# Optimization experiments

Hardware: AMD Instinct MI355X
Metric: run time of the kernel (lower is better)

Reference implementation:

```python
import jax, jax.numpy as jnp
import numpy as np

EPS = 1e-5

def layer_norm(x, g, b):
    mu = jnp.mean(x, axis=-1, keepdims=True)
    var = jnp.mean(jnp.square(x - mu), axis=-1, keepdims=True)
    return (x - mu) * jax.lax.rsqrt(var + EPS) * g + b

def setup_inputs() -> dict:
    key = jax.random.key(0)
    ks = jax.random.split(key, 8)
    B, T, D, H = 8, 2048, 32, 4
    hd = D // H
    s = 0.05
    return {
        "x": jax.random.normal(ks[0], (B, T, D), jnp.float32),
        "Wq": jax.random.normal(ks[1], (H, D, hd), jnp.float32) * s,
        "Wk": jax.random.normal(ks[2], (H, D, hd), jnp.float32) * s,
        "Wv": jax.random.normal(ks[3], (H, D, hd), jnp.float32) * s,
        "Wproj": jax.random.normal(ks[4], (D, D), jnp.float32) * s,
        "bproj": jnp.zeros((D,), jnp.float32),
        "ln1_g": jnp.ones((D,), jnp.float32),
        "ln1_b": jnp.zeros((D,), jnp.float32),
        "W1": jax.random.normal(ks[5], (D, 4 * D), jnp.float32) * s,
        "b1": jnp.zeros((4 * D,), jnp.float32),
        "W2": jax.random.normal(ks[6], (4 * D, D), jnp.float32) * s,
        "b2": jnp.zeros((D,), jnp.float32),
        "ln2_g": jnp.ones((D,), jnp.float32),
        "ln2_b": jnp.zeros((D,), jnp.float32),
    }

def reference(x, Wq, Wk, Wv, Wproj, bproj, ln1_g, ln1_b, W1, b1, W2, b2, ln2_g, ln2_b):
    B, T, D = x.shape
    H, _, hd = Wq.shape
    scale = hd ** -0.5
    # NOTE: original block normalizes first, and the residual uses the NORMALIZED x
    h = layer_norm(x, ln1_g, ln1_b)                      # (B,T,D)
    q = jnp.einsum('btd,hdk->bhtk', h, Wq)
    k = jnp.einsum('btd,hdk->bhtk', h, Wk)
    v = jnp.einsum('btd,hdk->bhtk', h, Wv)
    scores = jnp.einsum('bhtk,bhsk->bhts', q, k) * scale  # (B,H,T,T)
    mask = jnp.tril(jnp.ones((T, T), bool))
    scores = jnp.where(mask, scores, -jnp.inf)
    attn = jax.nn.softmax(scores, axis=-1)               # dropout = identity (eval)
    o = jnp.einsum('bhts,bhsk->bhtk', attn, v)           # (B,H,T,hd)
    o = o.transpose(0, 2, 1, 3).reshape(B, T, D)         # concat heads, head0 first
    x1 = h + o @ Wproj + bproj
    h2 = layer_norm(x1, ln2_g, ln2_b)
    ff = jax.nn.relu(h2 @ W1 + b1) @ W2 + b2             # dropout = identity (eval)
    return h2 + ff
```

## Files before the change

### kernel.cpp

```cpp
#include <hip/hip_runtime.h>
#include <math.h>

#define BB 8
#define TT 2048
#define DD 32
#define HH 4
#define HD 8
#define NROWS (BB*TT)
#define LNEPS 1e-5f

#if __has_builtin(__builtin_amdgcn_exp2f)
#define EXP2F(x) __builtin_amdgcn_exp2f(x)
#else
#define EXP2F(x) __expf(0.6931471805599453f*(x))
#endif

typedef _Float16 h2 __attribute__((ext_vector_type(2)));
typedef _Float16 h4v __attribute__((ext_vector_type(4)));
typedef float f4v __attribute__((ext_vector_type(4)));
struct KH { h2 a, b, c, d; };
union F4H { float4 f; KH k; };

static __device__ __forceinline__ h2 pkrtz(float a, float b) {
    return __builtin_bit_cast(h2, __builtin_amdgcn_cvt_pkrtz(a, b));
}
static __device__ __forceinline__ unsigned pkrtz_u(float a, float b) {
    return __builtin_bit_cast(unsigned, __builtin_amdgcn_cvt_pkrtz(a, b));
}
static __device__ __forceinline__ unsigned short f16u(float x) {
    return __builtin_bit_cast(unsigned short, (_Float16)x);
}

__global__ __launch_bounds__(256) void k_ln_qkv(
    const float* __restrict__ x,
    const float* __restrict__ Wq, const float* __restrict__ Wk, const float* __restrict__ Wv,
    const float* __restrict__ g, const float* __restrict__ b,
    float* __restrict__ h, float* __restrict__ qh,
    float* __restrict__ Kh, float* __restrict__ Vt)
{
    __shared__ float sW[3*HH*264];
    __shared__ float sg[DD], sb[DD];
    for (int i = threadIdx.x; i < HH*DD*HD; i += 256) {
        int hd_ = i >> 8, off = i & 255;
        sW[hd_*264 + off]              = Wq[i];
        sW[(4+hd_)*264 + off]          = Wk[i];
        sW[(8+hd_)*264 + off]          = Wv[i];
    }
    if (threadIdx.x < DD) { sg[threadIdx.x] = g[threadIdx.x]; sb[threadIdx.x] = b[threadIdx.x]; }
    __syncthreads();

    int idx = blockIdx.x * 256 + threadIdx.x;
    int r   = idx >> 3;
    int sub = idx & 7;
    int hh  = sub & 3;
    int dh  = sub >> 2;
    int bb  = r >> 11, tt = r & 2047;

    float xr[16];
    {
        const float4* xp = (const float4*)(x + (size_t)r * DD + dh*16);
        float4 t0 = xp[0], t1 = xp[1], t2 = xp[2], t3 = xp[3];
        xr[0]=t0.x; xr[1]=t0.y; xr[2]=t0.z; xr[3]=t0.w;
        xr[4]=t1.x; xr[5]=t1.y; xr[6]=t1.z; xr[7]=t1.w;
        xr[8]=t2.x; xr[9]=t2.y; xr[10]=t2.z; xr[11]=t2.w;
        xr[12]=t3.x; xr[13]=t3.y; xr[14]=t3.z; xr[15]=t3.w;
    }
    float s1 = 0.f;
    #pragma unroll
    for (int i = 0; i < 16; ++i) s1 += xr[i];
    s1 += __shfl_xor(s1, 4, 64);
    float mu = s1 * (1.f/DD);
    float sq = 0.f;
    #pragma unroll
    for (int i = 0; i < 16; ++i) { float d = xr[i]-mu; sq += d*d; }
    sq += __shfl_xor(sq, 4, 64);
    float rs = rsqrtf(sq * (1.f/DD) + LNEPS);

    float hr[16];
    #pragma unroll
    for (int i = 0; i < 16; ++i) hr[i] = (xr[i]-mu)*rs*sg[dh*16+i] + sb[dh*16+i];

    {
        float4* hp = (float4*)(h + (size_t)r * DD + dh*16);
        hp[0]=make_float4(hr[0],hr[1],hr[2],hr[3]);
        hp[1]=make_float4(hr[4],hr[5],hr[6],hr[7]);
        hp[2]=make_float4(hr[8],hr[9],hr[10],hr[11]);
        hp[3]=make_float4(hr[12],hr[13],hr[14],hr[15]);
    }

    const float* wq = sW + hh*264 + dh*128;
    const float* wk = sW + (4+hh)*264 + dh*128;
    const float* wv = sW + (8+hh)*264 + dh*128;
    float qa[HD], ka[HD], va[HD];
    #pragma unroll
    for (int k2 = 0; k2 < HD; ++k2) { qa[k2]=0.f; ka[k2]=0.f; va[k2]=0.f; }
    #pragma unroll
    for (int d = 0; d < 16; ++d) {
        float hv = hr[d];
        const float4* wq4 = (const float4*)(wq + d*8);
        const float4* wk4 = (const float4*)(wk + d*8);
        const float4* wv4 = (const float4*)(wv + d*8);
        float4 a0 = wq4[0], a1 = wq4[1];
        float4 b0 = wk4[0], b1 = wk4[1];
        float4 c0 = wv4[0], c1 = wv4[1];
        qa[0]=fmaf(hv,a0.x,qa[0]); qa[1]=fmaf(hv,a0.y,qa[1]); qa[2]=fmaf(hv,a0.z,qa[2]); qa[3]=fmaf(hv,a0.w,qa[3]);
        qa[4]=fmaf(hv,a1.x,qa[4]); qa[5]=fmaf(hv,a1.y,qa[5]); qa[6]=fmaf(hv,a1.z,qa[6]); qa[7]=fmaf(hv,a1.w,qa[7]);
        ka[0]=fmaf(hv,b0.x,ka[0]); ka[1]=fmaf(hv,b0.y,ka[1]); ka[2]=fmaf(hv,b0.z,ka[2]); ka[3]=fmaf(hv,b0.w,ka[3]);
        ka[4]=fmaf(hv,b1.x,ka[4]); ka[5]=fmaf(hv,b1.y,ka[5]); ka[6]=fmaf(hv,b1.z,ka[6]); ka[7]=fmaf(hv,b1.w,ka[7]);
        va[0]=fmaf(hv,c0.x,va[0]); va[1]=fmaf(hv,c0.y,va[1]); va[2]=fmaf(hv,c0.z,va[2]); va[3]=fmaf(hv,c0.w,va[3]);
        va[4]=fmaf(hv,c1.x,va[4]); va[5]=fmaf(hv,c1.y,va[5]); va[6]=fmaf(hv,c1.z,va[6]); va[7]=fmaf(hv,c1.w,va[7]);
    }
    #pragma unroll
    for (int k2 = 0; k2 < HD; ++k2) {
        qa[k2] += __shfl_xor(qa[k2], 4, 64);
        ka[k2] += __shfl_xor(ka[k2], 4, 64);
        va[k2] += __shfl_xor(va[k2], 4, 64);
    }

    const float SCL = 0.35355339059327373f * 1.4426950408889634f;
    size_t key = (size_t)(bb*HH + hh)*TT + tt;
    unsigned short* vtb = (unsigned short*)Vt + (size_t)(bb*HH + hh)*8*TT + tt;
    if (dh == 0) {
        F4H u;
        u.k.a = pkrtz(qa[0]*SCL, qa[1]*SCL);
        u.k.b = pkrtz(qa[2]*SCL, qa[3]*SCL);
        u.k.c = pkrtz(qa[4]*SCL, qa[5]*SCL);
        u.k.d = pkrtz(qa[6]*SCL, qa[7]*SCL);
        *(float4*)(qh + key*4) = u.f;
        vtb[(size_t)0*TT] = f16u(va[0]);
        vtb[(size_t)1*TT] = f16u(va[1]);
        vtb[(size_t)2*TT] = f16u(va[2]);
        vtb[(size_t)3*TT] = f16u(va[3]);
    } else {
        F4H u;
        u.k.a = pkrtz(ka[0], ka[1]);
        u.k.b = pkrtz(ka[2], ka[3]);
        u.k.c = pkrtz(ka[4], ka[5]);
        u.k.d = pkrtz(ka[6], ka[7]);
        *(float4*)(Kh + key*4) = u.f;
        vtb[(size_t)4*TT] = f16u(va[4]);
        vtb[(size_t)5*TT] = f16u(va[5]);
        vtb[(size_t)6*TT] = f16u(va[6]);
        vtb[(size_t)7*TT] = f16u(va[7]);
    }
}

__global__ __launch_bounds__(256) void k_attn(
    const float* __restrict__ qh, const float* __restrict__ Kh,
    const float* __restrict__ Vt, float* __restrict__ o)
{
    __shared__ char lds[2][2048];
    const int tid  = threadIdx.x;
    const int wave = tid >> 6;
    const int lane = tid & 63;
    const int g    = lane >> 4;
    const int qi   = lane & 15;
    const int bh   = blockIdx.x & 31;
    const int qblk = 31 - (int)(blockIdx.x >> 5);
    const int qb   = qblk << 6;
    const int wq0  = qb + (wave << 4);
    const int ntiles = qblk + 1;

    const float4*  KbF = (const float4*)Kh + (size_t)bh * TT;
    const ushort*  VtU = (const ushort*)Vt + (size_t)bh * 8 * TT;

    h4v qf;
    {
        uint2 qraw = make_uint2(0u, 0u);
        if (g < 2)
            qraw = *(const uint2*)((const ushort*)qh + ((size_t)bh*TT + wq0 + qi)*8 + (size_t)(g<<2));
        qf = __builtin_bit_cast(h4v, qraw);
    }

    f4v acc = {0.f, 0.f, 0.f, 0.f};
    float m = 0.f, l = 0.f;

    float4 st = make_float4(0.f,0.f,0.f,0.f);
    if (tid < 64) {
        st = KbF[tid];
    } else if (tid < 128) {
        int t2 = tid - 64, d = t2 >> 3, seg = (t2 & 7) ^ d;
        st = *(const float4*)(VtU + (size_t)d*TT + (seg << 3));
    }
    if (tid < 64)       *(float4*)(&lds[0][0] + tid*16) = st;
    else if (tid < 128) *(float4*)(&lds[0][0] + 1024 + (tid-64)*16) = st;
    __syncthreads();

    int buf = 0;
    for (int t = 0; t < ntiles; ++t) {
        const int tb = t << 6;
        float4 nx = make_float4(0.f,0.f,0.f,0.f);
        const bool more = (t + 1 < ntiles);
        if (more) {
            const int nb = (t + 1) << 6;
            if (tid < 64) nx = KbF[nb + tid];
            else if (tid < 128) {
                int t2 = tid - 64, d = t2 >> 3, seg = (t2 & 7) ^ d;
                nx = *(const float4*)(VtU + (size_t)d*TT + nb + (seg << 3));
            }
        }
        const char* smK = &lds[buf][0];
        const char* smV = &lds[buf][0] + 1024;
        #pragma unroll
        for (int c = 0; c < 4; ++c) {
            const int s0 = tb + (c << 4);
            if (s0 > wq0) continue;
            const bool diag = (s0 == wq0);

            uint2 kraw = *(const uint2*)(smK + ((c<<4) + qi)*16 + ((g&1)<<3));
            if (g >= 2) { kraw.x = 0u; kraw.y = 0u; }
            h4v kf = __builtin_bit_cast(h4v, kraw);

            const int d7 = lane & 7;
            uint2 vraw = *(const uint2*)(smV + d7*128 + (((c<<5) + (g<<3)) ^ (d7<<4)));
            h4v vf = __builtin_bit_cast(h4v, vraw);

            f4v Z = {0.f,0.f,0.f,0.f};
            f4v S = __builtin_amdgcn_mfma_f32_16x16x16f16(kf, qf, Z, 0, 0, 0);

            float dd[4];
            #pragma unroll
            for (int r = 0; r < 4; ++r) {
                float v = S[r];
                if (diag && ((g<<2) + r > qi)) v = -1e30f;
                dd[r] = v;
            }
            float pm = fmaxf(fmaxf(dd[0], dd[1]), fmaxf(dd[2], dd[3]));
            pm = fmaxf(pm, __shfl_xor(pm, 16, 64));
            pm = fmaxf(pm, __shfl_xor(pm, 32, 64));
            if (__builtin_expect(__any(pm - m > 8.f), 0)) {
                float mn = fmaxf(m, pm);
                float cr = EXP2F(m - mn);
                l *= cr;
                #pragma unroll
                for (int r = 0; r < 4; ++r) {
                    float c4 = __shfl(cr, (g<<2) + r, 64);
                    acc[r] *= c4;
                }
                m = mn;
            }
            float p0 = EXP2F(dd[0] - m);
            float p1 = EXP2F(dd[1] - m);
            float p2 = EXP2F(dd[2] - m);
            float p3 = EXP2F(dd[3] - m);
            l += (p0 + p1) + (p2 + p3);
            uint2 pu; pu.x = pkrtz_u(p0, p1); pu.y = pkrtz_u(p2, p3);
            h4v pf = __builtin_bit_cast(h4v, pu);
            acc = __builtin_amdgcn_mfma_f32_16x16x16f16(pf, vf, acc, 0, 0, 0);
        }
        if (more) {
            if (tid < 64)       *(float4*)(&lds[buf^1][0] + tid*16) = nx;
            else if (tid < 128) *(float4*)(&lds[buf^1][0] + 1024 + (tid-64)*16) = nx;
        }
        __syncthreads();
        buf ^= 1;
    }

    l += __shfl_xor(l, 16, 64);
    l += __shfl_xor(l, 32, 64);
    float Linv = 1.f / l;
    float Li[4];
    #pragma unroll
    for (int r = 0; r < 4; ++r) Li[r] = __shfl(Linv, (g<<2) + r, 64);
    if (qi < HD) {
        float* ob = o + ((size_t)bh*TT + wq0)*HD + qi;
        #pragma unroll
        for (int r = 0; r < 4; ++r)
            ob[(size_t)((g<<2) + r) * HD] = acc[r] * Li[r];
    }
}

__global__ __launch_bounds__(256) void k_proj_ffn(
    const float* __restrict__ h, const float* __restrict__ o,
    const float* __restrict__ Wproj, const float* __restrict__ bproj,
    const float* __restrict__ W1, const float* __restrict__ b1,
    const float* __restrict__ W2, const float* __restrict__ b2,
    const float* __restrict__ g2, const float* __restrict__ bt2,
    float* __restrict__ out)
{
    __shared__ float sWp[DD*36], sW1T[4*DD*36], sW2[4*DD*36];
    __shared__ float sbp[DD], sb1[4*DD], sb2[DD], sg2[DD], sbt2[DD];
    for (int i = threadIdx.x; i < DD*DD; i += 256)      sWp [(i>>5)*36 + (i&31)] = Wproj[i];
    for (int i = threadIdx.x; i < DD*4*DD; i += 256) {
        sW1T[(i&127)*36 + (i>>7)] = W1[i];
        sW2 [(i>>5)*36 + (i&31)]  = W2[i];
    }
    if (threadIdx.x < DD) {
        sbp[threadIdx.x]  = bproj[threadIdx.x];
        sb2[threadIdx.x]  = b2[threadIdx.x];
        sg2[threadIdx.x]  = g2[threadIdx.x];
        sbt2[threadIdx.x] = bt2[threadIdx.x];
    }
    if (threadIdx.x < 4*DD) sb1[threadIdx.x] = b1[threadIdx.x];
    __syncthreads();

    int idx = blockIdx.x * 256 + threadIdx.x;
    int r   = idx >> 3;
    int sub = idx & 7;
    int bb  = r >> 11, tt = r & 2047;

    float o4[4];
    #pragma unroll
    for (int mm = 0; mm < 4; ++mm)
        o4[mm] = o[((size_t)(bb*HH + mm)*TT + tt) * HD + sub];

    float x1[DD];
    #pragma unroll
    for (int d = 0; d < DD; ++d) x1[d] = 0.f;
    #pragma unroll
    for (int mm = 0; mm < 4; ++mm) {
        const float4* wr = (const float4*)&sWp[(sub + 8*mm)*36];
        float ov = o4[mm];
        #pragma unroll
        for (int dc = 0; dc < 8; ++dc) {
            float4 w4 = wr[dc];
            x1[4*dc]   = fmaf(ov, w4.x, x1[4*dc]);
            x1[4*dc+1] = fmaf(ov, w4.y, x1[4*dc+1]);
            x1[4*dc+2] = fmaf(ov, w4.z, x1[4*dc+2]);
            x1[4*dc+3] = fmaf(ov, w4.w, x1[4*dc+3]);
        }
    }
    #pragma unroll
    for (int d = 0; d < DD; ++d) {
        x1[d] += __shfl_xor(x1[d], 1, 64);
        x1[d] += __shfl_xor(x1[d], 2, 64);
        x1[d] += __shfl_xor(x1[d], 4, 64);
    }
    {
        const float4* hp = (const float4*)(h + (size_t)r * DD);
        #pragma unroll
        for (int dc = 0; dc < 8; ++dc) {
            float4 h4 = hp[dc];
            x1[4*dc]   += h4.x + sbp[4*dc];
            x1[4*dc+1] += h4.y + sbp[4*dc+1];
            x1[4*dc+2] += h4.z + sbp[4*dc+2];
            x1[4*dc+3] += h4.w + sbp[4*dc+3];
        }
    }
    float mu = 0.f;
    #pragma unroll
    for (int d = 0; d < DD; ++d) mu += x1[d];
    mu *= (1.f/DD);
    float var = 0.f;
    #pragma unroll
    for (int d = 0; d < DD; ++d) { float dl = x1[d]-mu; var += dl*dl; }
    var *= (1.f/DD);
    float rs = rsqrtf(var + LNEPS);
    float h2v[DD];
    #pragma unroll
    for (int d = 0; d < DD; ++d) h2v[d] = (x1[d]-mu)*rs*sg2[d] + sbt2[d];

    float outp[DD];
    #pragma unroll
    for (int d = 0; d < DD; ++d) outp[d] = 0.f;
    #pragma unroll
    for (int mm = 0; mm < 16; ++mm) {
        int j = sub + 8*mm;
        const float4* w1r = (const float4*)&sW1T[j*36];
        float a = sb1[j];
        #pragma unroll
        for (int dc = 0; dc < 8; ++dc) {
            float4 w4 = w1r[dc];
            a = fmaf(h2v[4*dc], w4.x, a);
            a = fmaf(h2v[4*dc+1], w4.y, a);
            a = fmaf(h2v[4*dc+2], w4.z, a);
            a = fmaf(h2v[4*dc+3], w4.w, a);
        }
        a = fmaxf(a, 0.f);
        const float4* w2r = (const float4*)&sW2[j*36];
        #pragma unroll
        for (int dc = 0; dc < 8; ++dc) {
            float4 w4 = w2r[dc];
            outp[4*dc]   = fmaf(a, w4.x, outp[4*dc]);
            outp[4*dc+1] = fmaf(a, w4.y, outp[4*dc+1]);
            outp[4*dc+2] = fmaf(a, w4.z, outp[4*dc+2]);
            outp[4*dc+3] = fmaf(a, w4.w, outp[4*dc+3]);
        }
    }
    if (sub == 0) {
        #pragma unroll
        for (int d = 0; d < DD; ++d) outp[d] += h2v[d] + sb2[d];
    }
    float t1[16];
    #pragma unroll
    for (int i = 0; i < 16; ++i) {
        bool hi = (sub & 4) != 0;
        float send = hi ? outp[i] : outp[i+16];
        float recv = __shfl_xor(send, 4, 64);
        t1[i] = (hi ? outp[i+16] : outp[i]) + recv;
    }
    float t2[8];
    #pragma unroll
    for (int i = 0; i < 8; ++i) {
        bool hi = (sub & 2) != 0;
        float send = hi ? t1[i] : t1[i+8];
        float recv = __shfl_xor(send, 2, 64);
        t2[i] = (hi ? t1[i+8] : t1[i]) + recv;
    }
    float w0[4];
    #pragma unroll
    for (int i = 0; i < 4; ++i) {
        bool hi = (sub & 1) != 0;
        float send = hi ? t2[i] : t2[i+4];
        float recv = __shfl_xor(send, 1, 64);
        w0[i] = (hi ? t2[i+4] : t2[i]) + recv;
    }
    *(float4*)(out + (size_t)r * DD + sub*4) = make_float4(w0[0], w0[1], w0[2], w0[3]);
}

extern "C" void kernel_launch(void* const* d_in, const int* in_sizes, int n_in,
                              void* d_out, int out_size, void* d_ws, size_t ws_size,
                              hipStream_t stream) {
    const float* x     = (const float*)d_in[0];
    const float* Wq    = (const float*)d_in[1];
    const float* Wk    = (const float*)d_in[2];
    const float* Wv    = (const float*)d_in[3];
    const float* Wproj = (const float*)d_in[4];
    const float* bproj = (const float*)d_in[5];
    const float* ln1_g = (const float*)d_in[6];
    const float* ln1_b = (const float*)d_in[7];
    const float* W1    = (const float*)d_in[8];
    const float* b1    = (const float*)d_in[9];
    const float* W2    = (const float*)d_in[10];
    const float* b2    = (const float*)d_in[11];
    const float* ln2_g = (const float*)d_in[12];
    const float* ln2_b = (const float*)d_in[13];
    float* out = (float*)d_out;

    const size_t N = (size_t)NROWS * DD;
    const size_t K = (size_t)BB*HH*TT*4;
    float* ws = (float*)d_ws;
    float* h  = ws;
    float* qh = ws + N;
    float* Kh = ws + N + K;
    float* Vt = ws + N + 2*K;
    float* o  = ws + N + 3*K;

    k_ln_qkv  <<<512, 256, 0, stream>>>(x, Wq, Wk, Wv, ln1_g, ln1_b, h, qh, Kh, Vt);
    k_attn    <<<1024, 256, 0, stream>>>(qh, Kh, Vt, o);
    k_proj_ffn<<<512, 256, 0, stream>>>(h, o, Wproj, bproj, W1, b1, W2, b2, ln2_g, ln2_b, out);
}
```

Baseline: 137.9 us.

## Switch attention to 32x32 MFMA tiles with split-K waves and merged softmax

The attention kernel moves from 16x16x16 MFMA with half-wasted lanes to 32x32x8 for scores and 32x32x16 for P·V, so each wave handles 32 queries. The four waves now pair up: each pair shares a query group and alternates key tiles, then merges max, sum and partial outputs through LDS at the end. K and V are written in a new tiled, swizzled layout to match. The running max is folded into the MFMA accumulator input, and row sums use fdot2. This aims to reduce wasted MFMA work and softmax overhead per key, at the cost of a cross-wave merge and extra synchronisation.

```diff
diff --git a/kernel.cpp b/kernel.cpp
--- a/kernel.cpp
+++ b/kernel.cpp
@@ -17,7 +17,8 @@
 
 typedef _Float16 h2 __attribute__((ext_vector_type(2)));
 typedef _Float16 h4v __attribute__((ext_vector_type(4)));
-typedef float f4v __attribute__((ext_vector_type(4)));
+typedef _Float16 h8v __attribute__((ext_vector_type(8)));
+typedef float f32x16 __attribute__((ext_vector_type(16)));
 struct KH { h2 a, b, c, d; };
 union F4H { float4 f; KH k; };
 
@@ -30,6 +31,12 @@
 static __device__ __forceinline__ unsigned short f16u(float x) {
     return __builtin_bit_cast(unsigned short, (_Float16)x);
 }
+
+#if __has_builtin(__builtin_amdgcn_fdot2)
+#define DOT2(a,b,c) __builtin_amdgcn_fdot2((a),(b),(c),false)
+#else
+#define DOT2(a,b,c) fmaf((float)(a)[1],(float)(b)[1], fmaf((float)(a)[0],(float)(b)[0],(c)))
+#endif
 
 __global__ __launch_bounds__(256) void k_ln_qkv(
     const float* __restrict__ x,
@@ -119,7 +126,9 @@
 
     const float SCL = 0.35355339059327373f * 1.4426950408889634f;
     size_t key = (size_t)(bb*HH + hh)*TT + tt;
-    unsigned short* vtb = (unsigned short*)Vt + (size_t)(bb*HH + hh)*8*TT + tt;
+    char* Vb8 = (char*)Vt + (size_t)(bb*HH + hh)*32768;
+    int t6 = tt >> 6, tr = (tt & 63) << 1;
+    char* vrow = Vb8 + t6*128;
     if (dh == 0) {
         F4H u;
         u.k.a = pkrtz(qa[0]*SCL, qa[1]*SCL);
@@ -127,146 +136,204 @@
         u.k.c = pkrtz(qa[4]*SCL, qa[5]*SCL);
         u.k.d = pkrtz(qa[6]*SCL, qa[7]*SCL);
         *(float4*)(qh + key*4) = u.f;
-        vtb[(size_t)0*TT] = f16u(va[0]);
-        vtb[(size_t)1*TT] = f16u(va[1]);
-        vtb[(size_t)2*TT] = f16u(va[2]);
-        vtb[(size_t)3*TT] = f16u(va[3]);
+        *(unsigned short*)(vrow + 0*4096 + (tr ^ 0))   = f16u(va[0]);
+        *(unsigned short*)(vrow + 1*4096 + (tr ^ 16))  = f16u(va[1]);
+        *(unsigned short*)(vrow + 2*4096 + (tr ^ 32))  = f16u(va[2]);
+        *(unsigned short*)(vrow + 3*4096 + (tr ^ 48))  = f16u(va[3]);
     } else {
-        F4H u;
-        u.k.a = pkrtz(ka[0], ka[1]);
-        u.k.b = pkrtz(ka[2], ka[3]);
-        u.k.c = pkrtz(ka[4], ka[5]);
-        u.k.d = pkrtz(ka[6], ka[7]);
-        *(float4*)(Kh + key*4) = u.f;
-        vtb[(size_t)4*TT] = f16u(va[4]);
-        vtb[(size_t)5*TT] = f16u(va[5]);
-        vtb[(size_t)6*TT] = f16u(va[6]);
-        vtb[(size_t)7*TT] = f16u(va[7]);
-    }
+        char* Kb8 = (char*)Kh + (size_t)(bb*HH + hh)*32768;
+        uint2 k01; k01.x = pkrtz_u(ka[0],ka[1]); k01.y = pkrtz_u(ka[2],ka[3]);
+        uint2 k23; k23.x = pkrtz_u(ka[4],ka[5]); k23.y = pkrtz_u(ka[6],ka[7]);
+        *(uint2*)(Kb8 + (size_t)tt*8) = k01;
+        *(uint2*)(Kb8 + 16384 + (size_t)tt*8) = k23;
+        *(unsigned short*)(vrow + 4*4096 + (tr ^ 64))  = f16u(va[4]);
+        *(unsigned short*)(vrow + 5*4096 + (tr ^ 80))  = f16u(va[5]);
+        *(unsigned short*)(vrow + 6*4096 + (tr ^ 96))  = f16u(va[6]);
+        *(unsigned short*)(vrow + 7*4096 + (tr ^ 112)) = f16u(va[7]);
+    }
+}
+
+template<bool DIAG>
+__device__ __forceinline__ void do_chunk(
+    const char* __restrict__ smK, const char* __restrict__ smV,
+    int kc, int hi, int col, h4v qf,
+    float& m, float& l, f32x16& acc)
+{
+    uint2 kraw = *(const uint2*)(smK + hi*512 + (size_t)(kc + col)*8);
+    h4v kf = __builtin_bit_cast(h4v, kraw);
+    f32x16 cin;
+    #pragma unroll
+    for (int r2 = 0; r2 < 16; ++r2) cin[r2] = -m;
+    f32x16 S = __builtin_amdgcn_mfma_f32_32x32x8f16(kf, qf, cin, 0, 0, 0);
+    if (DIAG) {
+        #pragma unroll
+        for (int r2 = 0; r2 < 16; ++r2) {
+            int row = (r2&3) + 8*(r2>>2) + 4*hi;
+            if (row > col) S[r2] = -1e30f;
+        }
+    }
+    float pm = S[0];
+    #pragma unroll
+    for (int r2 = 1; r2 < 16; ++r2) pm = fmaxf(pm, S[r2]);
+    pm = fmaxf(pm, __shfl_xor(pm, 32, 64));
+    if (__builtin_expect(__any(pm > 8.f), 0)) {
+        float adj = fmaxf(pm, 0.f);
+        float cr  = EXP2F(-adj);
+        l *= cr;
+        #pragma unroll
+        for (int r2 = 0; r2 < 16; ++r2) {
+            int row = (r2&3) + 8*(r2>>2) + 4*hi;
+            acc[r2] *= __shfl(cr, row, 64);
+        }
+        #pragma unroll
+        for (int r2 = 0; r2 < 16; ++r2) S[r2] -= adj;
+        m += adj;
+    }
+    float p[16];
+    #pragma unroll
+    for (int r2 = 0; r2 < 16; ++r2) p[r2] = EXP2F(S[r2]);
+    unsigned pa_ = pkrtz_u(p[0],  p[1]);
+    unsigned pb_ = pkrtz_u(p[2],  p[3]);
+    unsigned pc_ = pkrtz_u(p[4],  p[5]);
+    unsigned pd_ = pkrtz_u(p[6],  p[7]);
+    unsigned pe_ = pkrtz_u(p[8],  p[9]);
+    unsigned pf_ = pkrtz_u(p[10], p[11]);
+    unsigned pg_ = pkrtz_u(p[12], p[13]);
+    unsigned ph_ = pkrtz_u(p[14], p[15]);
+    const h2 one2 = {(_Float16)1.f, (_Float16)1.f};
+    l = DOT2(__builtin_bit_cast(h2, pa_), one2, l);
+    l = DOT2(__builtin_bit_cast(h2, pb_), one2, l);
+    l = DOT2(__builtin_bit_cast(h2, pc_), one2, l);
+    l = DOT2(__builtin_bit_cast(h2, pd_), one2, l);
+    l = DOT2(__builtin_bit_cast(h2, pe_), one2, l);
+    l = DOT2(__builtin_bit_cast(h2, pf_), one2, l);
+    l = DOT2(__builtin_bit_cast(h2, pg_), one2, l);
+    l = DOT2(__builtin_bit_cast(h2, ph_), one2, l);
+    unsigned ra = (unsigned)__shfl_xor((int)pa_, 32, 64);
+    unsigned rb = (unsigned)__shfl_xor((int)pb_, 32, 64);
+    unsigned rc = (unsigned)__shfl_xor((int)pc_, 32, 64);
+    unsigned rd = (unsigned)__shfl_xor((int)pd_, 32, 64);
+    unsigned re = (unsigned)__shfl_xor((int)pe_, 32, 64);
+    unsigned rf = (unsigned)__shfl_xor((int)pf_, 32, 64);
+    unsigned rg = (unsigned)__shfl_xor((int)pg_, 32, 64);
+    unsigned rh = (unsigned)__shfl_xor((int)ph_, 32, 64);
+    bool H = (hi != 0);
+    uint4 A0 = { H?rc:pa_, H?rd:pb_, H?pc_:ra, H?pd_:rb };
+    uint4 A1 = { H?rg:pe_, H?rh:pf_, H?pg_:re, H?ph_:rf };
+    int d7 = col & 7;
+    const char* vrow = smV + d7*128;
+    uint4 v0 = *(const uint4*)(vrow + ((((kc + hi*8) << 1)) ^ (d7 << 4)));
+    uint4 v1 = *(const uint4*)(vrow + ((((kc + 16 + hi*8) << 1)) ^ (d7 << 4)));
+    acc = __builtin_amdgcn_mfma_f32_32x32x16_f16(
+        __builtin_bit_cast(h8v, A0), __builtin_bit_cast(h8v, v0), acc, 0, 0, 0);
+    acc = __builtin_amdgcn_mfma_f32_32x32x16_f16(
+        __builtin_bit_cast(h8v, A1), __builtin_bit_cast(h8v, v1), acc, 0, 0, 0);
 }
 
 __global__ __launch_bounds__(256) void k_attn(
     const float* __restrict__ qh, const float* __restrict__ Kh,
     const float* __restrict__ Vt, float* __restrict__ o)
 {
-    __shared__ char lds[2][2048];
+    __shared__ char lds[7168];
     const int tid  = threadIdx.x;
     const int wave = tid >> 6;
     const int lane = tid & 63;
-    const int g    = lane >> 4;
-    const int qi   = lane & 15;
+    const int hi   = lane >> 5;
+    const int col  = lane & 31;
+    const int qg   = wave >> 1;
+    const int kh   = wave & 1;
     const int bh   = blockIdx.x & 31;
     const int qblk = 31 - (int)(blockIdx.x >> 5);
     const int qb   = qblk << 6;
-    const int wq0  = qb + (wave << 4);
+    const int wq0  = qb + (qg << 5);
     const int ntiles = qblk + 1;
 
-    const float4*  KbF = (const float4*)Kh + (size_t)bh * TT;
-    const ushort*  VtU = (const ushort*)Vt + (size_t)bh * 8 * TT;
-
-    h4v qf;
+    const char* Kg = (const char*)Kh + (size_t)bh * 32768;
+    const char* Vg = (const char*)Vt + (size_t)bh * 32768;
+    const char* Qg = (const char*)qh + (size_t)bh * 32768 + (size_t)wq0 * 16;
+
+    h4v qf = __builtin_bit_cast(h4v, *(const uint2*)(Qg + col*16 + hi*8));
+
+    f32x16 acc;
+    #pragma unroll
+    for (int r2 = 0; r2 < 16; ++r2) acc[r2] = 0.f;
+    float m = 0.f, l = 0.f;
+
     {
-        uint2 qraw = make_uint2(0u, 0u);
-        if (g < 2)
-            qraw = *(const uint2*)((const ushort*)qh + ((size_t)bh*TT + wq0 + qi)*8 + (size_t)(g<<2));
-        qf = __builtin_bit_cast(h4v, qraw);
-    }
-
-    f4v acc = {0.f, 0.f, 0.f, 0.f};
-    float m = 0.f, l = 0.f;
-
-    float4 st = make_float4(0.f,0.f,0.f,0.f);
-    if (tid < 64) {
-        st = KbF[tid];
-    } else if (tid < 128) {
-        int t2 = tid - 64, d = t2 >> 3, seg = (t2 & 7) ^ d;
-        st = *(const float4*)(VtU + (size_t)d*TT + (seg << 3));
-    }
-    if (tid < 64)       *(float4*)(&lds[0][0] + tid*16) = st;
-    else if (tid < 128) *(float4*)(&lds[0][0] + 1024 + (tid-64)*16) = st;
+        uint4 st;
+        if (tid < 64)       st = *(const uint4*)(Kg + (tid>>5)*16384 + (size_t)(tid&31)*16);
+        else if (tid < 128) { int ix = tid-64; st = *(const uint4*)(Vg + (ix>>3)*4096 + (ix&7)*16); }
+        if (tid < 64)       *(uint4*)(&lds[0] + (tid>>5)*512 + (tid&31)*16) = st;
+        else if (tid < 128) *(uint4*)(&lds[0] + 1024 + (tid-64)*16) = st;
+    }
     __syncthreads();
 
     int buf = 0;
     for (int t = 0; t < ntiles; ++t) {
-        const int tb = t << 6;
-        float4 nx = make_float4(0.f,0.f,0.f,0.f);
+        uint4 nx;
         const bool more = (t + 1 < ntiles);
         if (more) {
-            const int nb = (t + 1) << 6;
-            if (tid < 64) nx = KbF[nb + tid];
-            else if (tid < 128) {
-                int t2 = tid - 64, d = t2 >> 3, seg = (t2 & 7) ^ d;
-                nx = *(const float4*)(VtU + (size_t)d*TT + nb + (seg << 3));
+            if (tid < 64)       nx = *(const uint4*)(Kg + (tid>>5)*16384 + (t+1)*512 + (tid&31)*16);
+            else if (tid < 128) { int ix = tid-64; nx = *(const uint4*)(Vg + (ix>>3)*4096 + (t+1)*128 + (ix&7)*16); }
+        }
+        if ((t & 1) == kh) {
+            const int tb = t << 6;
+            const char* smK = &lds[buf*2048];
+            const char* smV = smK + 1024;
+            if (tb <= wq0) {
+                if (tb == wq0) do_chunk<true >(smK, smV, 0, hi, col, qf, m, l, acc);
+                else           do_chunk<false>(smK, smV, 0, hi, col, qf, m, l, acc);
+                if (tb + 32 <= wq0) {
+                    if (tb + 32 == wq0) do_chunk<true >(smK, smV, 32, hi, col, qf, m, l, acc);
+                    else                do_chunk<false>(smK, smV, 32, hi, col, qf, m, l, acc);
+                }
             }
         }
-        const char* smK = &lds[buf][0];
-        const char* smV = &lds[buf][0] + 1024;
-        #pragma unroll
-        for (int c = 0; c < 4; ++c) {
-            const int s0 = tb + (c << 4);
-            if (s0 > wq0) continue;
-            const bool diag = (s0 == wq0);
-
-            uint2 kraw = *(const uint2*)(smK + ((c<<4) + qi)*16 + ((g&1)<<3));
-            if (g >= 2) { kraw.x = 0u; kraw.y = 0u; }
-            h4v kf = __builtin_bit_cast(h4v, kraw);
-
-            const int d7 = lane & 7;
-            uint2 vraw = *(const uint2*)(smV + d7*128 + (((c<<5) + (g<<3)) ^ (d7<<4)));
-            h4v vf = __builtin_bit_cast(h4v, vraw);
-
-            f4v Z = {0.f,0.f,0.f,0.f};
-            f4v S = __builtin_amdgcn_mfma_f32_16x16x16f16(kf, qf, Z, 0, 0, 0);
-
-            float dd[4];
-            #pragma unroll
-            for (int r = 0; r < 4; ++r) {
-                float v = S[r];
-                if (diag && ((g<<2) + r > qi)) v = -1e30f;
-                dd[r] = v;
-            }
-            float pm = fmaxf(fmaxf(dd[0], dd[1]), fmaxf(dd[2], dd[3]));
-            pm = fmaxf(pm, __shfl_xor(pm, 16, 64));
-            pm = fmaxf(pm, __shfl_xor(pm, 32, 64));
-            if (__builtin_expect(__any(pm - m > 8.f), 0)) {
-                float mn = fmaxf(m, pm);
-                float cr = EXP2F(m - mn);
-                l *= cr;
-                #pragma unroll
-                for (int r = 0; r < 4; ++r) {
-                    float c4 = __shfl(cr, (g<<2) + r, 64);
-                    acc[r] *= c4;
-                }
-                m = mn;
-            }
-            float p0 = EXP2F(dd[0] - m);
-            float p1 = EXP2F(dd[1] - m);
-            float p2 = EXP2F(dd[2] - m);
-            float p3 = EXP2F(dd[3] - m);
-            l += (p0 + p1) + (p2 + p3);
-            uint2 pu; pu.x = pkrtz_u(p0, p1); pu.y = pkrtz_u(p2, p3);
-            h4v pf = __builtin_bit_cast(h4v, pu);
-            acc = __builtin_amdgcn_mfma_f32_16x16x16f16(pf, vf, acc, 0, 0, 0);
-        }
         if (more) {
-            if (tid < 64)       *(float4*)(&lds[buf^1][0] + tid*16) = nx;
-            else if (tid < 128) *(float4*)(&lds[buf^1][0] + 1024 + (tid-64)*16) = nx;
+            if (tid < 64)       *(uint4*)(&lds[(buf^1)*2048] + (tid>>5)*512 + (tid&31)*16) = nx;
+            else if (tid < 128) *(uint4*)(&lds[(buf^1)*2048] + 1024 + (tid-64)*16) = nx;
         }
         __syncthreads();
         buf ^= 1;
     }
 
-    l += __shfl_xor(l, 16, 64);
     l += __shfl_xor(l, 32, 64);
-    float Linv = 1.f / l;
-    float Li[4];
-    #pragma unroll
-    for (int r = 0; r < 4; ++r) Li[r] = __shfl(Linv, (g<<2) + r, 64);
-    if (qi < HD) {
-        float* ob = o + ((size_t)bh*TT + wq0)*HD + qi;
-        #pragma unroll
-        for (int r = 0; r < 4; ++r)
-            ob[(size_t)((g<<2) + r) * HD] = acc[r] * Li[r];
+    float* mb = (float*)&lds[4096];
+    float* lb = (float*)&lds[4608];
+    float* ob = (float*)&lds[5120];
+    if (lane < 32) {
+        mb[(kh<<6) + (qg<<5) + col] = m;
+        lb[(kh<<6) + (qg<<5) + col] = l;
+    }
+    __syncthreads();
+    float mo = mb[((kh^1)<<6) + (qg<<5) + col];
+    float lo = lb[((kh^1)<<6) + (qg<<5) + col];
+    float M  = fmaxf(m, mo);
+    float fs = EXP2F(m - M);
+    float L  = l * fs + lo * EXP2F(mo - M);
+    float Linv = 1.f / L;
+    float fr[16], Lr[16];
+    #pragma unroll
+    for (int r2 = 0; r2 < 16; ++r2) {
+        int row = (r2&3) + 8*(r2>>2) + 4*hi;
+        fr[r2] = __shfl(fs,   row, 64);
+        Lr[r2] = __shfl(Linv, row, 64);
+    }
+    if (kh == 1 && col < HD) {
+        #pragma unroll
+        for (int r2 = 0; r2 < 16; ++r2) {
+            int row = (r2&3) + 8*(r2>>2) + 4*hi;
+            ob[(qg<<8) + (row<<3) + col] = acc[r2] * fr[r2];
+        }
+    }
+    __syncthreads();
+    if (kh == 0 && col < HD) {
+        float* og = o + ((size_t)bh*TT + wq0)*HD + col;
+        #pragma unroll
+        for (int r2 = 0; r2 < 16; ++r2) {
+            int row = (r2&3) + 8*(r2>>2) + 4*hi;
+            og[(size_t)row * HD] = (acc[r2]*fr[r2] + ob[(qg<<8) + (row<<3) + col]) * Lr[r2];
+        }
     }
 }
 
@@ -384,26 +451,26 @@
     float t1[16];
     #pragma unroll
     for (int i = 0; i < 16; ++i) {
-        bool hi = (sub & 4) != 0;
-        float send = hi ? outp[i] : outp[i+16];
+        bool hib = (sub & 4) != 0;
+        float send = hib ? outp[i] : outp[i+16];
         float recv = __shfl_xor(send, 4, 64);
-        t1[i] = (hi ? outp[i+16] : outp[i]) + recv;
+        t1[i] = (hib ? outp[i+16] : outp[i]) + recv;
     }
     float t2[8];
     #pragma unroll
     for (int i = 0; i < 8; ++i) {
-        bool hi = (sub & 2) != 0;
-        float send = hi ? t1[i] : t1[i+8];
+        bool hib = (sub & 2) != 0;
+        float send = hib ? t1[i] : t1[i+8];
         float recv = __shfl_xor(send, 2, 64);
-        t2[i] = (hi ? t1[i+8] : t1[i]) + recv;
+        t2[i] = (hib ? t1[i+8] : t1[i]) + recv;
     }
     float w0[4];
     #pragma unroll
     for (int i = 0; i < 4; ++i) {
-        bool hi = (sub & 1) != 0;
-        float send = hi ? t2[i] : t2[i+4];
+        bool hib = (sub & 1) != 0;
+        float send = hib ? t2[i] : t2[i+4];
         float recv = __shfl_xor(send, 1, 64);
-        w0[i] = (hi ? t2[i+4] : t2[i]) + recv;
+        w0[i] = (hib ? t2[i+4] : t2[i]) + recv;
     }
     *(float4*)(out + (size_t)r * DD + sub*4) = make_float4(w0[0], w0[1], w0[2], w0[3]);
 }
```

Result: no change. 137.7 us (-0.2%).
